# Kernel optimization log

Measured on AMD Instinct MI355X. Metric: run time of the kernel, lower is better.

The kernel has to match this reference:

```python
import jax, jax.numpy as jnp
import numpy as np

B, L, H, E, V = 32, 1024, 1024, 512, 8192

def setup_inputs() -> dict:
    key = jax.random.key(0)
    k1, k2, k3, k4 = jax.random.split(key, 4)
    x = jax.random.randint(k1, (B, L), 0, V)
    hidden = jnp.zeros((B, H), dtype=jnp.float32)  # equivalent to hidden=None path
    embedding = jax.random.normal(k2, (V, E), dtype=jnp.float32)
    W_h = jax.random.normal(k3, (E + H, H), dtype=jnp.float32) * 0.01
    b_h = jnp.zeros((H,), dtype=jnp.float32)
    W_o = jax.random.normal(k4, (H, V), dtype=jnp.float32) * 0.01
    b_o = jnp.zeros((V,), dtype=jnp.float32)
    return {"x": x, "hidden": hidden, "embedding": embedding,
            "W_h": W_h, "b_h": b_h, "W_o": W_o, "b_o": b_o}

def reference(x, hidden, embedding, W_h, b_h, W_o, b_o):
    # x: [B, L] int; hidden: [B, H]
    x_embed = embedding[x]                       # [B, L, E]
    x_tl = jnp.swapaxes(x_embed, 0, 1)           # [L, B, E] time-major

    def step(h, x_t):
        # concat + matmul + bias + tanh, one timestep
        combined = jnp.concatenate([x_t, h], axis=1)   # [B, E+H]
        h_new = jnp.tanh(combined @ W_h + b_h)         # [B, H]
        return h_new, h_new

    final_hidden, outs = jax.lax.scan(step, hidden, x_tl)  # outs: [L, B, H]
    output = jnp.swapaxes(outs, 0, 1)                       # [B, L, H]
    logits = output @ W_o + b_o                             # [B, L, V]
    return logits, final_hidden
```

## Files before the change

kernel.cpp:

```cpp
#include <hip/hip_runtime.h>
#include <hip/hip_bf16.h>

typedef unsigned short u16;
typedef unsigned int   u32;
typedef unsigned long long u64;
typedef __attribute__((ext_vector_type(8))) __bf16 bf16x8;
typedef __attribute__((ext_vector_type(4))) float   f32x4;

#define GLOAD16(gp, lp) __builtin_amdgcn_global_load_lds( \
    (__attribute__((address_space(1))) void*)(gp),        \
    (__attribute__((address_space(3))) void*)(lp), 16, 0, 0)

static __device__ __forceinline__ u16 f2bf(float f) {
  __bf16 b = (__bf16)f;
  return __builtin_bit_cast(u16, b);
}
static __device__ __forceinline__ f32x4 mfma16(bf16x8 a, bf16x8 b, f32x4 c) {
  return __builtin_amdgcn_mfma_f32_16x16x32_bf16(a, b, c, 0, 0, 0);
}
static __device__ __forceinline__ bf16x8 ald16(const u16* p) {
  union { u64 q[2]; bf16x8 v; } u;
  u.q[0] = __hip_atomic_load((const u64*)p,       __ATOMIC_RELAXED, __HIP_MEMORY_SCOPE_AGENT);
  u.q[1] = __hip_atomic_load((const u64*)(p + 4), __ATOMIC_RELAXED, __HIP_MEMORY_SCOPE_AGENT);
  return u.v;
}


__global__ __launch_bounds__(256) void k_cvt_emb(const float* __restrict__ s,
                                                 u16* __restrict__ d) {
  int i = (blockIdx.x * 256 + threadIdx.x) * 4;
  float4 v = *(const float4*)(s + i);
  d[i] = f2bf(v.x); d[i+1] = f2bf(v.y); d[i+2] = f2bf(v.z); d[i+3] = f2bf(v.w);
}

__global__ __launch_bounds__(256) void k_tr_wh(const float* __restrict__ Wh,
                                               u16* __restrict__ WhxT,
                                               u16* __restrict__ WhhT) {
  __shared__ float tile[32][33];
  int bx = blockIdx.x & 31;
  int be = blockIdx.x >> 5;
  int tx = threadIdx.x & 31, ty = threadIdx.x >> 5;
  #pragma unroll
  for (int s = 0; s < 32; s += 8)
    tile[ty + s][tx] = Wh[(size_t)(be*32 + ty + s) * 1024 + bx*32 + tx];
  __syncthreads();
  #pragma unroll
  for (int s = 0; s < 32; s += 8) {
    int e = be*32 + tx;
    int j = bx*32 + ty + s;
    u16 v = f2bf(tile[tx][ty + s]);
    if (e < 512) WhxT[(size_t)j * 512 + e] = v;
    else         WhhT[(size_t)j * 1024 + (e - 512)] = v;
  }
}

__global__ __launch_bounds__(256) void k_tr_wo(const float* __restrict__ Wo,
                                               u16* __restrict__ WoT) {
  __shared__ float tile[32][33];
  int bx = blockIdx.x & 255;
  int by = blockIdx.x >> 8;
  int tx = threadIdx.x & 31, ty = threadIdx.x >> 5;
  #pragma unroll
  for (int s = 0; s < 32; s += 8)
    tile[ty + s][tx] = Wo[(size_t)(by*32 + ty + s) * 8192 + bx*32 + tx];
  __syncthreads();
  #pragma unroll
  for (int s = 0; s < 32; s += 8)
    WoT[(size_t)(bx*32 + ty + s) * 1024 + by*32 + tx] = f2bf(tile[tx][ty + s]);
}

__global__ __launch_bounds__(256) void k_init(const float* __restrict__ hid,
                                              u16* __restrict__ ring,
                                              unsigned* __restrict__ flags) {
  int i = blockIdx.x * 256 + threadIdx.x;
  ring[i] = f2bf(hid[i]);
  if (blockIdx.x < 8) flags[i] = 0;
}

__global__ __launch_bounds__(256) void k_xpart(const int* __restrict__ xq,
                                               const u16* __restrict__ embB,
                                               const u16* __restrict__ WhxT,
                                               const float* __restrict__ bh,
                                               float* __restrict__ xpart) {
  __shared__ __align__(16) u16 As[128 * 32];
  __shared__ __align__(16) u16 Bs[128 * 32];
  __shared__ int sx[128];
  int bid = blockIdx.x;
  int cpx = gridDim.x >> 3;
  int swz = (bid & 7) * cpx + (bid >> 3);
  int tm = (swz >> 3) * 128, tn = (swz & 7) * 128;
  int tid = threadIdx.x, lane = tid & 63, w = tid >> 6;
  int wm = (w >> 1) * 64, wn = (w & 1) * 64;
  if (tid < 128) sx[tid] = xq[tm + tid];
  __syncthreads();
  int r0 = tid >> 2, sub = tid & 3;
  const u16* ga0 = embB + (size_t)sx[r0] * 512 + sub * 8;
  const u16* ga1 = embB + (size_t)sx[64 + r0] * 512 + sub * 8;
  const u16* gb0 = WhxT + (size_t)(tn + r0) * 512 + sub * 8;
  const u16* gb1 = WhxT + (size_t)(tn + 64 + r0) * 512 + sub * 8;
  f32x4 acc[4][4] = {};
  int rl = lane & 15, kb = (lane >> 4) * 8;
  for (int kt = 0; kt < 16; ++kt) {
    int k0 = kt * 32;
    __syncthreads();
    GLOAD16(ga0 + k0, As + w * 512);
    GLOAD16(ga1 + k0, As + 2048 + w * 512);
    GLOAD16(gb0 + k0, Bs + w * 512);
    GLOAD16(gb1 + k0, Bs + 2048 + w * 512);
    __syncthreads();
    bf16x8 af[4], bf[4];
    #pragma unroll
    for (int mi = 0; mi < 4; mi++) af[mi] = *(const bf16x8*)&As[(wm + mi*16 + rl) * 32 + kb];
    #pragma unroll
    for (int ni = 0; ni < 4; ni++) bf[ni] = *(const bf16x8*)&Bs[(wn + ni*16 + rl) * 32 + kb];
    #pragma unroll
    for (int mi = 0; mi < 4; mi++)
      #pragma unroll
      for (int ni = 0; ni < 4; ni++)
        acc[mi][ni] = mfma16(af[mi], bf[ni], acc[mi][ni]);
  }
  int rq = (lane >> 4) << 2;
  #pragma unroll
  for (int ni = 0; ni < 4; ni++) {
    int col = tn + wn + ni*16 + rl;
    float bias = bh[col];
    #pragma unroll
    for (int mi = 0; mi < 4; mi++) {
      int row = tm + wm + mi*16 + rq;
      #pragma unroll
      for (int r = 0; r < 4; r++)
        xpart[(size_t)(row + r) * 1024 + col] = acc[mi][ni][r] + bias;
    }
  }
}

__global__ __launch_bounds__(256) void k_rnn(const u16* __restrict__ WhhT,
                                             const float* __restrict__ xpart,
                                             u16* __restrict__ ring,
                                             float* __restrict__ hfinal,
                                             unsigned* __restrict__ flags) {
  __shared__ __align__(16) float psh[2048];
  int bid = blockIdx.x, tid = threadIdx.x, lane = tid & 63, w = tid >> 6;
  int jbase = bid * 16;
  const int rl = lane & 15;
  const int kbase = w * 256 + ((lane >> 4) << 3);
  bf16x8 Wreg[8];
  #pragma unroll
  for (int ki = 0; ki < 8; ++ki)
    Wreg[ki] = *(const bf16x8*)&WhhT[(size_t)(jbase + rl) * 1024 + kbase + ki * 32];
  const bool red = (tid < 128);
  int b = 0, jq = 0, mi = 0, lsrc = 0, rg = 0;
  float4 xpre = make_float4(0.f, 0.f, 0.f, 0.f);
  if (red) {
    b = tid >> 2; jq = (tid & 3) << 2;
    mi = b >> 4;
    int bb = b & 15;
    lsrc = (bb >> 2) << 4;
    rg = bb & 3;
    xpre = *(const float4*)&xpart[(size_t)(b * 1024 + 0) * 1024 + jbase + jq];
  }
  for (int t = 0; t < 1024; ++t) {
    const u16* hprev = ring + (size_t)t * 32768;
    bf16x8 ha[16];
    #pragma unroll
    for (int ki = 0; ki < 8; ++ki) {
      int k = kbase + ki * 32;
      ha[ki*2 + 0] = *(const bf16x8*)&hprev[(size_t)rl * 1024 + k];
      ha[ki*2 + 1] = *(const bf16x8*)&hprev[(size_t)(16 + rl) * 1024 + k];
    }
    f32x4 acc0 = {0.f, 0.f, 0.f, 0.f}, acc1 = {0.f, 0.f, 0.f, 0.f};
    #pragma unroll
    for (int ki = 0; ki < 8; ++ki) {
      acc0 = mfma16(ha[ki*2 + 0], Wreg[ki], acc0);
      acc1 = mfma16(ha[ki*2 + 1], Wreg[ki], acc1);
    }
    *(f32x4*)&psh[((w * 2 + 0) * 64 + lane) * 4] = acc0;
    *(f32x4*)&psh[((w * 2 + 1) * 64 + lane) * 4] = acc1;
    __syncthreads();
    if (red) {
      float s0 = 0.f, s1 = 0.f, s2 = 0.f, s3 = 0.f;
      #pragma unroll
      for (int ww = 0; ww < 4; ++ww) {
        const float* pp = &psh[((ww * 2 + mi) * 64) * 4];
        s0 += pp[(lsrc + jq + 0) * 4 + rg];
        s1 += pp[(lsrc + jq + 1) * 4 + rg];
        s2 += pp[(lsrc + jq + 2) * 4 + rg];
        s3 += pp[(lsrc + jq + 3) * 4 + rg];
      }
      float v0 = tanhf(s0 + xpre.x);
      float v1 = tanhf(s1 + xpre.y);
      float v2 = tanhf(s2 + xpre.z);
      float v3 = tanhf(s3 + xpre.w);
      u32 lo = (u32)f2bf(v0) | ((u32)f2bf(v1) << 16);
      u32 hi = (u32)f2bf(v2) | ((u32)f2bf(v3) << 16);
      u64 hv = (u64)lo | ((u64)hi << 32);
      __hip_atomic_store((u64*)(ring + (size_t)(t + 1) * 32768 + b * 1024 + jbase + jq),
                         hv, __ATOMIC_RELAXED, __HIP_MEMORY_SCOPE_AGENT);
      if (t == 1023)
        *(float4*)&hfinal[b * 1024 + jbase + jq] = make_float4(v0, v1, v2, v3);
    }
    if (t < 1023) {
      asm volatile("s_waitcnt vmcnt(0)" ::: "memory");
      __syncthreads();
      if (tid == 0)
        __hip_atomic_store(&flags[bid * 32], (unsigned)(t + 1),
                           __ATOMIC_RELAXED, __HIP_MEMORY_SCOPE_AGENT);
      if (red)
        xpre = *(const float4*)&xpart[((size_t)(b * 1024 + (t + 1))) * 1024 + jbase + jq];
      if (w == 0) {
        while (__hip_atomic_load(&flags[lane * 32], __ATOMIC_RELAXED,
                                 __HIP_MEMORY_SCOPE_AGENT) < (unsigned)(t + 1)) { }
      }
      __syncthreads();
    } else {
      asm volatile("s_waitcnt vmcnt(0)" ::: "memory");
      __syncthreads();
      if (tid == 0)
        __hip_atomic_store(&flags[bid * 32], 1024u,
                           __ATOMIC_RELAXED, __HIP_MEMORY_SCOPE_AGENT);
    }
  }
}

__global__ __launch_bounds__(256) void k_logits(const u16* __restrict__ A,
                                                const u16* __restrict__ BT,
                                                const float* __restrict__ bo,
                                                float* __restrict__ C,
                                                const unsigned* __restrict__ flags) {
  __shared__ __align__(16) u16 As[128 * 32];
  __shared__ __align__(16) u16 Bs[128 * 32];
  int bid = blockIdx.x;
  int tIdx = bid >> 6, vIdx = bid & 63;
  int tm = tIdx * 128, tn = vIdx * 128;
  int tid = threadIdx.x, lane = tid & 63, w = tid >> 6;
  if (tid < 64) {
    unsigned tgt = (unsigned)(tIdx * 4 + 4);
    const unsigned* fp = flags + tid * 32;
    for (;;) {
      unsigned v = __hip_atomic_load(fp, __ATOMIC_RELAXED, __HIP_MEMORY_SCOPE_AGENT);
      if (!__any((int)(v < tgt))) break;
      __builtin_amdgcn_s_sleep(32);
    }
  }
  __syncthreads();
  int wm = (w >> 1) * 64, wn = (w & 1) * 64;
  int r0 = tid >> 2, sub = tid & 3;
  const u16* ga0 = A + (size_t)(tm + r0) * 1024 + sub * 8;
  const u16* ga1 = A + (size_t)(tm + 64 + r0) * 1024 + sub * 8;
  const u16* gb0 = BT + (size_t)(tn + r0) * 1024 + sub * 8;
  const u16* gb1 = BT + (size_t)(tn + 64 + r0) * 1024 + sub * 8;
  f32x4 acc[4][4] = {};
  int rl = lane & 15, kb = (lane >> 4) * 8;
  for (int kt = 0; kt < 32; ++kt) {
    int k0 = kt * 32;
    __syncthreads();
    GLOAD16(ga0 + k0, As + w * 512);
    GLOAD16(ga1 + k0, As + 2048 + w * 512);
    GLOAD16(gb0 + k0, Bs + w * 512);
    GLOAD16(gb1 + k0, Bs + 2048 + w * 512);
    __syncthreads();
    bf16x8 af[4], bf[4];
    #pragma unroll
    for (int mi = 0; mi < 4; mi++) af[mi] = *(const bf16x8*)&As[(wm + mi*16 + rl) * 32 + kb];
    #pragma unroll
    for (int ni = 0; ni < 4; ni++) bf[ni] = *(const bf16x8*)&Bs[(wn + ni*16 + rl) * 32 + kb];
    #pragma unroll
    for (int mi = 0; mi < 4; mi++)
      #pragma unroll
      for (int ni = 0; ni < 4; ni++)
        acc[mi][ni] = mfma16(af[mi], bf[ni], acc[mi][ni]);
  }
  int rq = (lane >> 4) << 2;
  #pragma unroll
  for (int ni = 0; ni < 4; ni++) {
    int col = tn + wn + ni*16 + rl;
    float bias = bo[col];
    #pragma unroll
    for (int mi = 0; mi < 4; mi++) {
      int row = tm + wm + mi*16 + rq;
      #pragma unroll
      for (int r = 0; r < 4; r++) {
        int m = row + r;
        size_t orow = (size_t)(((m & 31) << 10) | (m >> 5));
        C[orow * 8192 + col] = acc[mi][ni][r] + bias;
      }
    }
  }
}

extern "C" void kernel_launch(void* const* d_in, const int* in_sizes, int n_in,
                              void* d_out, int out_size, void* d_ws, size_t ws_size,
                              hipStream_t stream) {
  const int*   x   = (const int*)  d_in[0];
  const float* hid = (const float*)d_in[1];
  const float* emb = (const float*)d_in[2];
  const float* Wh  = (const float*)d_in[3];
  const float* bh  = (const float*)d_in[4];
  const float* Wo  = (const float*)d_in[5];
  const float* bo  = (const float*)d_in[6];
  float* logits = (float*)d_out;
  float* hfinal = logits + (size_t)32768 * 8192;

  char* ws = (char*)d_ws;
  size_t off = 0;
  auto alloc = [&](size_t bytes) {
    char* p = ws + off;
    off += (bytes + 255) & ~(size_t)255;
    return p;
  };
  u16*   embB  = (u16*)  alloc((size_t)8192 * 512 * 2);
  u16*   WhxT  = (u16*)  alloc((size_t)1024 * 512 * 2);
  u16*   WhhT  = (u16*)  alloc((size_t)1024 * 1024 * 2);
  u16*   WoT   = (u16*)  alloc((size_t)8192 * 1024 * 2);
  float* xpart = (float*)alloc((size_t)32768 * 1024 * 4);
  u16*   ring  = (u16*)  alloc((size_t)1025 * 32768 * 2);
  unsigned* flags = (unsigned*)alloc(8192);
  (void)ws_size; (void)in_sizes; (void)n_in; (void)out_size;

  k_cvt_emb<<<4096, 256, 0, stream>>>(emb, embB);
  k_tr_wh  <<<1536, 256, 0, stream>>>(Wh, WhxT, WhhT);
  k_tr_wo  <<<8192, 256, 0, stream>>>(Wo, WoT);
  k_init   <<<128,  256, 0, stream>>>(hid, ring, flags);
  k_xpart  <<<2048, 256, 0, stream>>>(x, embB, WhxT, bh, xpart);
  k_rnn    <<<64,   256, 0, stream>>>(WhhT, xpart, ring, hfinal, flags);
  k_logits <<<16384,256, 0, stream>>>(ring + 32768, WoT, bo, logits, flags);
}
```

Before: 5.004 ms.

## Fuse RNN recurrence and logits GEMM into one persistent kernel with work queue

Merges the recurrent kernel and the output-projection GEMM into a single launch. The first 64 blocks run the recurrence, and the remaining blocks pull 128x64 logits tiles from an atomic counter and wait on per-block timestep flags. Previously the logits kernel could only start after the recurrence finished, because both were launched on the same stream. Now the GEMM and the large logits writes can overlap the latency-bound scan. The risks are that concurrent GEMM traffic and the spinning waiter blocks slow the recurrence, and that the design relies on the queue counter being zeroed and on all 64 recurrence blocks being co-resident.

```diff
diff --git a/kernel.cpp b/kernel.cpp
--- a/kernel.cpp
+++ b/kernel.cpp
@@ -17,12 +17,6 @@
 }
 static __device__ __forceinline__ f32x4 mfma16(bf16x8 a, bf16x8 b, f32x4 c) {
   return __builtin_amdgcn_mfma_f32_16x16x32_bf16(a, b, c, 0, 0, 0);
-}
-static __device__ __forceinline__ bf16x8 ald16(const u16* p) {
-  union { u64 q[2]; bf16x8 v; } u;
-  u.q[0] = __hip_atomic_load((const u64*)p,       __ATOMIC_RELAXED, __HIP_MEMORY_SCOPE_AGENT);
-  u.q[1] = __hip_atomic_load((const u64*)(p + 4), __ATOMIC_RELAXED, __HIP_MEMORY_SCOPE_AGENT);
-  return u.v;
 }
 
 
@@ -134,155 +128,165 @@
   }
 }
 
-__global__ __launch_bounds__(256) void k_rnn(const u16* __restrict__ WhhT,
-                                             const float* __restrict__ xpart,
-                                             u16* __restrict__ ring,
-                                             float* __restrict__ hfinal,
-                                             unsigned* __restrict__ flags) {
-  __shared__ __align__(16) float psh[2048];
-  int bid = blockIdx.x, tid = threadIdx.x, lane = tid & 63, w = tid >> 6;
-  int jbase = bid * 16;
-  const int rl = lane & 15;
-  const int kbase = w * 256 + ((lane >> 4) << 3);
-  bf16x8 Wreg[8];
-  #pragma unroll
-  for (int ki = 0; ki < 8; ++ki)
-    Wreg[ki] = *(const bf16x8*)&WhhT[(size_t)(jbase + rl) * 1024 + kbase + ki * 32];
-  const bool red = (tid < 128);
-  int b = 0, jq = 0, mi = 0, lsrc = 0, rg = 0;
-  float4 xpre = make_float4(0.f, 0.f, 0.f, 0.f);
-  if (red) {
-    b = tid >> 2; jq = (tid & 3) << 2;
-    mi = b >> 4;
-    int bb = b & 15;
-    lsrc = (bb >> 2) << 4;
-    rg = bb & 3;
-    xpre = *(const float4*)&xpart[(size_t)(b * 1024 + 0) * 1024 + jbase + jq];
-  }
-  for (int t = 0; t < 1024; ++t) {
-    const u16* hprev = ring + (size_t)t * 32768;
-    bf16x8 ha[16];
-    #pragma unroll
-    for (int ki = 0; ki < 8; ++ki) {
-      int k = kbase + ki * 32;
-      ha[ki*2 + 0] = *(const bf16x8*)&hprev[(size_t)rl * 1024 + k];
-      ha[ki*2 + 1] = *(const bf16x8*)&hprev[(size_t)(16 + rl) * 1024 + k];
-    }
-    f32x4 acc0 = {0.f, 0.f, 0.f, 0.f}, acc1 = {0.f, 0.f, 0.f, 0.f};
-    #pragma unroll
-    for (int ki = 0; ki < 8; ++ki) {
-      acc0 = mfma16(ha[ki*2 + 0], Wreg[ki], acc0);
-      acc1 = mfma16(ha[ki*2 + 1], Wreg[ki], acc1);
-    }
-    *(f32x4*)&psh[((w * 2 + 0) * 64 + lane) * 4] = acc0;
-    *(f32x4*)&psh[((w * 2 + 1) * 64 + lane) * 4] = acc1;
+__global__ __launch_bounds__(256, 4) void k_fused(const u16* __restrict__ WhhT,
+                                                  const float* __restrict__ xpart,
+                                                  u16* __restrict__ ring,
+                                                  float* __restrict__ hfinal,
+                                                  unsigned* flags,
+                                                  const u16* __restrict__ WoT,
+                                                  const float* __restrict__ bo,
+                                                  float* __restrict__ C) {
+  __shared__ __align__(16) u16 smem[6144];
+  __shared__ int sq;
+  const int tid = threadIdx.x, lane = tid & 63, w = tid >> 6;
+
+  if (blockIdx.x < 64) {
+    float* psh = (float*)smem;
+    int bid = blockIdx.x;
+    int jbase = bid * 16;
+    const int rl = lane & 15;
+    const int kbase = w * 256 + ((lane >> 4) << 3);
+    bf16x8 Wreg[8];
+    #pragma unroll
+    for (int ki = 0; ki < 8; ++ki)
+      Wreg[ki] = *(const bf16x8*)&WhhT[(size_t)(jbase + rl) * 1024 + kbase + ki * 32];
+    const bool red = (tid < 128);
+    int b = 0, jq = 0, mi = 0, lsrc = 0, rg = 0;
+    float4 xpre = make_float4(0.f, 0.f, 0.f, 0.f);
+    if (red) {
+      b = tid >> 2; jq = (tid & 3) << 2;
+      mi = b >> 4;
+      int bb = b & 15;
+      lsrc = (bb >> 2) << 4;
+      rg = bb & 3;
+      xpre = *(const float4*)&xpart[(size_t)(b * 1024 + 0) * 1024 + jbase + jq];
+    }
+    for (int t = 0; t < 1024; ++t) {
+      const u16* hprev = ring + (size_t)t * 32768;
+      bf16x8 ha[16];
+      #pragma unroll
+      for (int ki = 0; ki < 8; ++ki) {
+        int k = kbase + ki * 32;
+        ha[ki*2 + 0] = *(const bf16x8*)&hprev[(size_t)rl * 1024 + k];
+        ha[ki*2 + 1] = *(const bf16x8*)&hprev[(size_t)(16 + rl) * 1024 + k];
+      }
+      f32x4 acc0 = {0.f, 0.f, 0.f, 0.f}, acc1 = {0.f, 0.f, 0.f, 0.f};
+      #pragma unroll
+      for (int ki = 0; ki < 8; ++ki) {
+        acc0 = mfma16(ha[ki*2 + 0], Wreg[ki], acc0);
+        acc1 = mfma16(ha[ki*2 + 1], Wreg[ki], acc1);
+      }
+      *(f32x4*)&psh[((w * 2 + 0) * 64 + lane) * 4] = acc0;
+      *(f32x4*)&psh[((w * 2 + 1) * 64 + lane) * 4] = acc1;
+      __syncthreads();
+      if (red) {
+        float s0 = 0.f, s1 = 0.f, s2 = 0.f, s3 = 0.f;
+        #pragma unroll
+        for (int ww = 0; ww < 4; ++ww) {
+          const float* pp = &psh[((ww * 2 + mi) * 64) * 4];
+          s0 += pp[(lsrc + jq + 0) * 4 + rg];
+          s1 += pp[(lsrc + jq + 1) * 4 + rg];
+          s2 += pp[(lsrc + jq + 2) * 4 + rg];
+          s3 += pp[(lsrc + jq + 3) * 4 + rg];
+        }
+        float v0 = tanhf(s0 + xpre.x);
+        float v1 = tanhf(s1 + xpre.y);
+        float v2 = tanhf(s2 + xpre.z);
+        float v3 = tanhf(s3 + xpre.w);
+        u32 lo = (u32)f2bf(v0) | ((u32)f2bf(v1) << 16);
+        u32 hi = (u32)f2bf(v2) | ((u32)f2bf(v3) << 16);
+        u64 hv = (u64)lo | ((u64)hi << 32);
+        __hip_atomic_store((u64*)(ring + (size_t)(t + 1) * 32768 + b * 1024 + jbase + jq),
+                           hv, __ATOMIC_RELAXED, __HIP_MEMORY_SCOPE_AGENT);
+        if (t == 1023)
+          *(float4*)&hfinal[b * 1024 + jbase + jq] = make_float4(v0, v1, v2, v3);
+      }
+      if (t < 1023) {
+        asm volatile("s_waitcnt vmcnt(0)" ::: "memory");
+        __syncthreads();
+        if (tid == 0)
+          __hip_atomic_store(&flags[bid * 32], (unsigned)(t + 1),
+                             __ATOMIC_RELAXED, __HIP_MEMORY_SCOPE_AGENT);
+        if (red)
+          xpre = *(const float4*)&xpart[((size_t)(b * 1024 + (t + 1))) * 1024 + jbase + jq];
+        if (w == 0) {
+          while (__hip_atomic_load(&flags[lane * 32], __ATOMIC_RELAXED,
+                                   __HIP_MEMORY_SCOPE_AGENT) < (unsigned)(t + 1)) { }
+        }
+        __syncthreads();
+      } else {
+        asm volatile("s_waitcnt vmcnt(0)" ::: "memory");
+        __syncthreads();
+        if (tid == 0)
+          __hip_atomic_store(&flags[bid * 32], 1024u,
+                             __ATOMIC_RELAXED, __HIP_MEMORY_SCOPE_AGENT);
+      }
+    }
+    return;
+  }
+
+  u16* As = smem;
+  u16* Bs = smem + 4096;
+  unsigned* qctr = flags + 2047;
+  const u16* A = ring + 32768;
+  const int wm = (w >> 1) * 64, wn = (w & 1) * 32;
+  const int r0 = tid >> 2, sub = tid & 3;
+  const int rl = lane & 15, kb = (lane >> 4) * 8;
+  const int rq = (lane >> 4) << 2;
+  for (;;) {
+    if (tid == 0)
+      sq = (int)__hip_atomic_fetch_add(qctr, 1u, __ATOMIC_RELAXED,
+                                       __HIP_MEMORY_SCOPE_AGENT);
     __syncthreads();
-    if (red) {
-      float s0 = 0.f, s1 = 0.f, s2 = 0.f, s3 = 0.f;
-      #pragma unroll
-      for (int ww = 0; ww < 4; ++ww) {
-        const float* pp = &psh[((ww * 2 + mi) * 64) * 4];
-        s0 += pp[(lsrc + jq + 0) * 4 + rg];
-        s1 += pp[(lsrc + jq + 1) * 4 + rg];
-        s2 += pp[(lsrc + jq + 2) * 4 + rg];
-        s3 += pp[(lsrc + jq + 3) * 4 + rg];
-      }
-      float v0 = tanhf(s0 + xpre.x);
-      float v1 = tanhf(s1 + xpre.y);
-      float v2 = tanhf(s2 + xpre.z);
-      float v3 = tanhf(s3 + xpre.w);
-      u32 lo = (u32)f2bf(v0) | ((u32)f2bf(v1) << 16);
-      u32 hi = (u32)f2bf(v2) | ((u32)f2bf(v3) << 16);
-      u64 hv = (u64)lo | ((u64)hi << 32);
-      __hip_atomic_store((u64*)(ring + (size_t)(t + 1) * 32768 + b * 1024 + jbase + jq),
-                         hv, __ATOMIC_RELAXED, __HIP_MEMORY_SCOPE_AGENT);
-      if (t == 1023)
-        *(float4*)&hfinal[b * 1024 + jbase + jq] = make_float4(v0, v1, v2, v3);
-    }
-    if (t < 1023) {
-      asm volatile("s_waitcnt vmcnt(0)" ::: "memory");
+    const int q = sq;
+    if (q >= 32768) return;
+    const int tIdx = q >> 7, vIdx = q & 127;
+    const int tm = tIdx * 128, tn = vIdx * 64;
+    if (tid < 64) {
+      unsigned tgt = (unsigned)(tIdx * 4 + 4);
+      const unsigned* fp = flags + tid * 32;
+      for (;;) {
+        unsigned v = __hip_atomic_load(fp, __ATOMIC_RELAXED, __HIP_MEMORY_SCOPE_AGENT);
+        if (!__any((int)(v < tgt))) break;
+        __builtin_amdgcn_s_sleep(127);
+      }
+    }
+    __syncthreads();
+    const u16* ga0 = A + (size_t)(tm + r0) * 1024 + sub * 8;
+    const u16* ga1 = A + (size_t)(tm + 64 + r0) * 1024 + sub * 8;
+    const u16* gb0 = WoT + (size_t)(tn + r0) * 1024 + sub * 8;
+    f32x4 acc[4][2] = {};
+    for (int kt = 0; kt < 32; ++kt) {
+      int k0 = kt * 32;
       __syncthreads();
-      if (tid == 0)
-        __hip_atomic_store(&flags[bid * 32], (unsigned)(t + 1),
-                           __ATOMIC_RELAXED, __HIP_MEMORY_SCOPE_AGENT);
-      if (red)
-        xpre = *(const float4*)&xpart[((size_t)(b * 1024 + (t + 1))) * 1024 + jbase + jq];
-      if (w == 0) {
-        while (__hip_atomic_load(&flags[lane * 32], __ATOMIC_RELAXED,
-                                 __HIP_MEMORY_SCOPE_AGENT) < (unsigned)(t + 1)) { }
-      }
+      GLOAD16(ga0 + k0, As + w * 512);
+      GLOAD16(ga1 + k0, As + 2048 + w * 512);
+      GLOAD16(gb0 + k0, Bs + w * 512);
       __syncthreads();
-    } else {
-      asm volatile("s_waitcnt vmcnt(0)" ::: "memory");
-      __syncthreads();
-      if (tid == 0)
-        __hip_atomic_store(&flags[bid * 32], 1024u,
-                           __ATOMIC_RELAXED, __HIP_MEMORY_SCOPE_AGENT);
-    }
-  }
-}
-
-__global__ __launch_bounds__(256) void k_logits(const u16* __restrict__ A,
-                                                const u16* __restrict__ BT,
-                                                const float* __restrict__ bo,
-                                                float* __restrict__ C,
-                                                const unsigned* __restrict__ flags) {
-  __shared__ __align__(16) u16 As[128 * 32];
-  __shared__ __align__(16) u16 Bs[128 * 32];
-  int bid = blockIdx.x;
-  int tIdx = bid >> 6, vIdx = bid & 63;
-  int tm = tIdx * 128, tn = vIdx * 128;
-  int tid = threadIdx.x, lane = tid & 63, w = tid >> 6;
-  if (tid < 64) {
-    unsigned tgt = (unsigned)(tIdx * 4 + 4);
-    const unsigned* fp = flags + tid * 32;
-    for (;;) {
-      unsigned v = __hip_atomic_load(fp, __ATOMIC_RELAXED, __HIP_MEMORY_SCOPE_AGENT);
-      if (!__any((int)(v < tgt))) break;
-      __builtin_amdgcn_s_sleep(32);
-    }
-  }
-  __syncthreads();
-  int wm = (w >> 1) * 64, wn = (w & 1) * 64;
-  int r0 = tid >> 2, sub = tid & 3;
-  const u16* ga0 = A + (size_t)(tm + r0) * 1024 + sub * 8;
-  const u16* ga1 = A + (size_t)(tm + 64 + r0) * 1024 + sub * 8;
-  const u16* gb0 = BT + (size_t)(tn + r0) * 1024 + sub * 8;
-  const u16* gb1 = BT + (size_t)(tn + 64 + r0) * 1024 + sub * 8;
-  f32x4 acc[4][4] = {};
-  int rl = lane & 15, kb = (lane >> 4) * 8;
-  for (int kt = 0; kt < 32; ++kt) {
-    int k0 = kt * 32;
-    __syncthreads();
-    GLOAD16(ga0 + k0, As + w * 512);
-    GLOAD16(ga1 + k0, As + 2048 + w * 512);
-    GLOAD16(gb0 + k0, Bs + w * 512);
-    GLOAD16(gb1 + k0, Bs + 2048 + w * 512);
-    __syncthreads();
-    bf16x8 af[4], bf[4];
-    #pragma unroll
-    for (int mi = 0; mi < 4; mi++) af[mi] = *(const bf16x8*)&As[(wm + mi*16 + rl) * 32 + kb];
-    #pragma unroll
-    for (int ni = 0; ni < 4; ni++) bf[ni] = *(const bf16x8*)&Bs[(wn + ni*16 + rl) * 32 + kb];
-    #pragma unroll
-    for (int mi = 0; mi < 4; mi++)
-      #pragma unroll
-      for (int ni = 0; ni < 4; ni++)
-        acc[mi][ni] = mfma16(af[mi], bf[ni], acc[mi][ni]);
-  }
-  int rq = (lane >> 4) << 2;
-  #pragma unroll
-  for (int ni = 0; ni < 4; ni++) {
-    int col = tn + wn + ni*16 + rl;
-    float bias = bo[col];
-    #pragma unroll
-    for (int mi = 0; mi < 4; mi++) {
-      int row = tm + wm + mi*16 + rq;
-      #pragma unroll
-      for (int r = 0; r < 4; r++) {
-        int m = row + r;
-        size_t orow = (size_t)(((m & 31) << 10) | (m >> 5));
-        C[orow * 8192 + col] = acc[mi][ni][r] + bias;
+      bf16x8 af[4], bf[2];
+      #pragma unroll
+      for (int mi = 0; mi < 4; mi++) af[mi] = *(const bf16x8*)&As[(wm + mi*16 + rl) * 32 + kb];
+      #pragma unroll
+      for (int ni = 0; ni < 2; ni++) bf[ni] = *(const bf16x8*)&Bs[(wn + ni*16 + rl) * 32 + kb];
+      #pragma unroll
+      for (int mi = 0; mi < 4; mi++)
+        #pragma unroll
+        for (int ni = 0; ni < 2; ni++)
+          acc[mi][ni] = mfma16(af[mi], bf[ni], acc[mi][ni]);
+    }
+    #pragma unroll
+    for (int ni = 0; ni < 2; ni++) {
+      int col = tn + wn + ni*16 + rl;
+      float bias = bo[col];
+      #pragma unroll
+      for (int mi = 0; mi < 4; mi++) {
+        int row = tm + wm + mi*16 + rq;
+        #pragma unroll
+        for (int r = 0; r < 4; r++) {
+          int m = row + r;
+          size_t orow = (size_t)(((m & 31) << 10) | (m >> 5));
+          C[orow * 8192 + col] = acc[mi][ni][r] + bias;
+        }
       }
     }
   }
@@ -322,6 +326,6 @@
   k_tr_wo  <<<8192, 256, 0, stream>>>(Wo, WoT);
   k_init   <<<128,  256, 0, stream>>>(hid, ring, flags);
   k_xpart  <<<2048, 256, 0, stream>>>(x, embB, WhxT, bh, xpart);
-  k_rnn    <<<64,   256, 0, stream>>>(WhhT, xpart, ring, hfinal, flags);
-  k_logits <<<16384,256, 0, stream>>>(ring + 32768, WoT, bo, logits, flags);
-}
+  k_fused  <<<1024, 256, 0, stream>>>(WhhT, xpart, ring, hfinal, flags,
+                                      WoT, bo, logits);
+}
```

Measured after the change: 7.925 ms. 1.58x slower.
